# Performance work log

Measured on AMD Instinct MI355X. Metric: run time of the kernel, lower is better.

Reference implementation:

```python
import jax, jax.numpy as jnp
import numpy as np

TOP_K = 2


def setup_inputs() -> dict:
    key = jax.random.key(0)
    ks = jax.random.split(key, 6)
    B, T, H, E, F = 2, 2048, 1024, 8, 4096
    s1 = 1.0 / np.sqrt(H)
    s2 = 1.0 / np.sqrt(F)
    return {
        "hidden_states": jax.random.normal(ks[0], (B, T, H), dtype=jnp.float32),
        "router_w": jax.random.normal(ks[1], (E, H), dtype=jnp.float32) * s1,
        "w1": jax.random.normal(ks[2], (E, H, F), dtype=jnp.float32) * s1,
        "b1": jnp.zeros((E, F), dtype=jnp.float32),
        "w2": jax.random.normal(ks[3], (E, F, H), dtype=jnp.float32) * s2,
        "b2": jnp.zeros((E, H), dtype=jnp.float32),
    }


def reference(hidden_states, router_w, w1, b1, w2, b2):
    # hidden_states: [B,T,H]; router_w: [E,H]; w1: [E,H,F]; w2: [E,F,H]
    E = router_w.shape[0]
    K = TOP_K
    dt = hidden_states.dtype

    # Router
    router_logits = jnp.einsum("bth,eh->bte", hidden_states, router_w)  # [B,T,E]
    topk_values, topk_indices = jax.lax.top_k(router_logits, K)         # [B,T,K]
    topk_weights = jax.nn.softmax(topk_values.astype(jnp.float32), axis=-1).astype(dt)

    # Dense all-expert MLP (module computes every expert on every token)
    h_mid = jax.nn.gelu(
        jnp.einsum("bth,ehf->btef", hidden_states, w1) + b1, approximate=False
    )  # [B,T,E,F]
    expert_outputs = jnp.einsum("btef,efh->bteh", h_mid, w2) + b2  # [B,T,E,H]

    # Gather top-K expert outputs and combine
    topk_out = jnp.take_along_axis(expert_outputs, topk_indices[..., None], axis=2)  # [B,T,K,H]
    mixed_output = jnp.sum(topk_out * topk_weights[..., None], axis=2)  # [B,T,H]

    # Load-balancing aux loss
    router_probs = jax.nn.softmax(router_logits.astype(jnp.float32), axis=-1)
    P = router_probs.mean(axis=(0, 1))                       # [E]
    hard = jax.nn.one_hot(topk_indices, E, dtype=jnp.float32)  # [B,T,K,E]
    f = hard.mean(axis=(0, 1, 2))                            # [E]
    aux_loss = jnp.float32(E) * jnp.sum(f * P)

    # concept_mat is None in a fresh module -> statement loss is exactly 0
    statement_loss = jnp.float32(0.0)
    return mixed_output, aux_loss, statement_loss
```

## Files before the change

kernel.cpp:

```cpp
#include <hip/hip_runtime.h>


typedef unsigned short ushort_t;
typedef __attribute__((ext_vector_type(2))) float f32x2;
typedef __attribute__((ext_vector_type(4))) unsigned int u32x4;
typedef __attribute__((ext_vector_type(4))) unsigned short u16x4;
typedef __attribute__((ext_vector_type(4))) float f32x4;
typedef __attribute__((ext_vector_type(8))) __bf16 bf16x8;

#define NTOK 4096
#define HD   1024
#define FD   4096
#define NE   8
#define NKTOT 8192

__device__ __forceinline__ ushort_t f2bf(float f) {
  unsigned u = __builtin_bit_cast(unsigned, f);
  u += 0x7fffu + ((u >> 16) & 1u);
  return (ushort_t)(u >> 16);
}
__device__ __forceinline__ unsigned pk2(float a, float b) {
  unsigned r;
  asm("v_cvt_pk_bf16_f32 %0, %1, %2" : "=v"(r) : "v"(a), "v"(b));
  return r;
}
__device__ __forceinline__ float bf2f(ushort_t u) {
  unsigned v = ((unsigned)u) << 16;
  return __builtin_bit_cast(float, v);
}
__device__ __forceinline__ bf16x8 frag_ld(const void* p) {
  u32x4 v = *reinterpret_cast<const u32x4*>(p);
  return __builtin_bit_cast(bf16x8, v);
}

#define GLOAD16(g, l) __builtin_amdgcn_global_load_lds(                         \
    (const __attribute__((address_space(1))) unsigned int*)(g),                 \
    (__attribute__((address_space(3))) unsigned int*)(l), 16, 0, 0)

#define WAITLGKM() do { asm volatile("s_waitcnt lgkmcnt(0)" ::: "memory");      \
                        __builtin_amdgcn_sched_barrier(0); } while (0)
#define WAITVM0()  asm volatile("s_waitcnt vmcnt(0)" ::: "memory")
#define BARRIER() do { asm volatile("s_waitcnt lgkmcnt(0)" ::: "memory");       \
                       __builtin_amdgcn_s_barrier(); } while (0)

__global__ void init_k(int* counts) {
  if (threadIdx.x < NE) counts[threadIdx.x] = 0;
}

__global__ void convx_k(const float* __restrict__ src, ushort_t* __restrict__ dst) {
  const size_t i = ((size_t)blockIdx.x * 256 + threadIdx.x) * 4;
  const f32x4 v = *reinterpret_cast<const f32x4*>(src + i);
  u16x4 o;
  o.x = f2bf(v.x); o.y = f2bf(v.y); o.z = f2bf(v.z); o.w = f2bf(v.w);
  *reinterpret_cast<u16x4*>(dst + i) = o;
}

__global__ void router_k(const float* __restrict__ x, const float* __restrict__ rw,
                         float* __restrict__ tokP, int* __restrict__ counts,
                         int* __restrict__ tk_e, int* __restrict__ tk_s,
                         float* __restrict__ tk_w) {
  const int w = threadIdx.x >> 6, l = threadIdx.x & 63;
  const int t = blockIdx.x * 4 + w;
  const float* xr = x + (size_t)t * HD;
  float acc[NE];
#pragma unroll
  for (int e = 0; e < NE; ++e) acc[e] = 0.f;
  for (int it = 0; it < HD / 64; ++it) {
    const int h = l + it * 64;
    const float xv = xr[h];
#pragma unroll
    for (int e = 0; e < NE; ++e) acc[e] = fmaf(xv, rw[e * HD + h], acc[e]);
  }
#pragma unroll
  for (int e = 0; e < NE; ++e) {
#pragma unroll
    for (int s = 32; s > 0; s >>= 1) acc[e] += __shfl_xor(acc[e], s, 64);
  }
  float m = acc[0];
#pragma unroll
  for (int e = 1; e < NE; ++e) m = fmaxf(m, acc[e]);
  float ssum = 0.f;
  float p[NE];
#pragma unroll
  for (int e = 0; e < NE; ++e) { p[e] = expf(acc[e] - m); ssum += p[e]; }
  const float inv = 1.f / ssum;
  if (l < NE) tokP[(size_t)t * NE + l] = p[l] * inv;

  if (l == 0) {
    int i0 = 0; float v0 = acc[0];
#pragma unroll
    for (int e = 1; e < NE; ++e) if (acc[e] > v0) { v0 = acc[e]; i0 = e; }
    int i1 = -1; float v1 = -3.4e38f;
#pragma unroll
    for (int e = 0; e < NE; ++e) if (e != i0 && acc[e] > v1) { v1 = acc[e]; i1 = e; }
    const float w0 = 1.f / (1.f + expf(v1 - v0));
    const int s0 = atomicAdd(&counts[i0], 1);
    const int s1 = atomicAdd(&counts[i1], 1);
    tk_e[2 * t] = i0;     tk_s[2 * t] = s0;     tk_w[2 * t] = w0;
    tk_e[2 * t + 1] = i1; tk_s[2 * t + 1] = s1; tk_w[2 * t + 1] = 1.f - w0;
  }
}

__global__ void finalize_k(const float* __restrict__ tokP, const int* __restrict__ counts,
                           int* __restrict__ offsets, float* __restrict__ out_tail) {
  __shared__ float red[16][8];
  const int tid = threadIdx.x;
  f32x4 a0 = {0.f, 0.f, 0.f, 0.f}, a1 = {0.f, 0.f, 0.f, 0.f};
#pragma unroll
  for (int k = 0; k < 4; ++k) {
    const float* p = tokP + ((size_t)tid * 4 + k) * 8;
    a0 += *reinterpret_cast<const f32x4*>(p);
    a1 += *reinterpret_cast<const f32x4*>(p + 4);
  }
#pragma unroll
  for (int s = 1; s < 64; s <<= 1) {
#pragma unroll
    for (int c = 0; c < 4; ++c) {
      a0[c] += __shfl_xor(a0[c], s, 64);
      a1[c] += __shfl_xor(a1[c], s, 64);
    }
  }
  if ((tid & 63) == 0) {
    const int wv = tid >> 6;
#pragma unroll
    for (int c = 0; c < 4; ++c) { red[wv][c] = a0[c]; red[wv][4 + c] = a1[c]; }
  }
  __syncthreads();
  if (tid == 0) {
    float P[8];
    for (int c = 0; c < 8; ++c) {
      float s = 0.f;
      for (int q = 0; q < 16; ++q) s += red[q][c];
      P[c] = s * (1.f / NTOK);
    }
    int off = 0; float aux = 0.f;
    for (int q = 0; q < NE; ++q) { offsets[q] = off; off += counts[q]; }
    for (int q = 0; q < NE; ++q) aux += ((float)counts[q] / (float)NKTOT) * P[q];
    out_tail[0] = (float)NE * aux;
    out_tail[1] = 0.f;
  }
}

__global__ void build_slots_k(const int* __restrict__ tk_e, const int* __restrict__ tk_s,
                              const int* __restrict__ offsets, int* __restrict__ slot_token) {
  const int i = blockIdx.x * 256 + threadIdx.x;
  const int e = tk_e[i];
  slot_token[offsets[e] + tk_s[i]] = i >> 1;
}

template <bool IS_G1>
__global__ __launch_bounds__(256, 4) void moe_fused(
    const ushort_t* __restrict__ A, const float* __restrict__ W,
    const float* __restrict__ bias,
    const int* __restrict__ counts, const int* __restrict__ offsets,
    const int* __restrict__ slot_token,
    ushort_t* __restrict__ midout, ushort_t* __restrict__ ybuf) {
  constexpr int KDF = IS_G1 ? HD : FD;
  constexpr int WST = IS_G1 ? FD : HD;
  constexpr int NSTEP = IS_G1 ? 16 : 32;
  const int id = blockIdx.x;
  const int e = id & 7;
  const int q = id >> 3;
  const int ty = q % 10;
  const int r = q / 10;
  const int np = IS_G1 ? r : (r >> 1);
  const int ks = IS_G1 ? 0 : (r & 1);
  const int n0 = np * 128;
  const int KB = ks * 2048;
  const int cnt = counts[e];
  if (ty * 128 >= cnt) return;
  const int off = offsets[e];
  const int pos0 = off + ty * 128;
  const int rr = cnt - ty * 128;
  const int rows_rem = rr < 128 ? rr : 128;

  __shared__ __align__(16) ushort_t lds[16384];

  const int tid = threadIdx.x;
  const int w = tid >> 6, l = tid & 63;
  const int wr = w >> 1, wc = w & 1;

  const int sw = (((l & 7) ^ ((l >> 3) & 7)) << 4);
  const char* ab[4];
#pragma unroll
  for (int c = 0; c < 4; ++c) {
    const int row = c * 32 + w * 8 + (l >> 3);
    int pos = pos0 + row; if (pos > NKTOT - 1) pos = NKTOT - 1;
    const size_t ar = IS_G1 ? (size_t)slot_token[pos] : (size_t)pos;
    ab[c] = (const char*)A + (ar * KDF + KB) * 2 + sw;
  }

  const float* wB = W + (size_t)e * ((size_t)HD * FD) +
                    ((size_t)KB + 16 * w) * WST + n0 + 2 * l;

  f32x4 acc[4][4] = {};

  for (int t = 0; t < NSTEP; ++t) {
#pragma unroll
    for (int c = 0; c < 4; ++c)
      GLOAD16(ab[c] + t * 128, &lds[(c * 32 + w * 8) * 64]);
    f32x2 R[16];
    const float* p = wB + (size_t)(t * 64) * WST;
#pragma unroll
    for (int i = 0; i < 16; ++i)
      R[i] = *reinterpret_cast<const f32x2*>(p + (size_t)i * WST);
    WAITVM0();
    {
      ushort_t* d = &lds[8192 + (2 * l) * 64];
      const int k7 = l & 7;
      u32x4 v;
      v.x = pk2(R[0].x, R[1].x); v.y = pk2(R[2].x, R[3].x);
      v.z = pk2(R[4].x, R[5].x); v.w = pk2(R[6].x, R[7].x);
      *reinterpret_cast<u32x4*>(d + (((2 * w) ^ k7) << 3)) = v;
      v.x = pk2(R[8].x, R[9].x);  v.y = pk2(R[10].x, R[11].x);
      v.z = pk2(R[12].x, R[13].x); v.w = pk2(R[14].x, R[15].x);
      *reinterpret_cast<u32x4*>(d + (((2 * w + 1) ^ k7) << 3)) = v;
      ushort_t* d2 = d + 64;
      v.x = pk2(R[0].y, R[1].y); v.y = pk2(R[2].y, R[3].y);
      v.z = pk2(R[4].y, R[5].y); v.w = pk2(R[6].y, R[7].y);
      *reinterpret_cast<u32x4*>(d2 + (((2 * w) ^ k7) << 3)) = v;
      v.x = pk2(R[8].y, R[9].y);  v.y = pk2(R[10].y, R[11].y);
      v.z = pk2(R[12].y, R[13].y); v.w = pk2(R[14].y, R[15].y);
      *reinterpret_cast<u32x4*>(d2 + (((2 * w + 1) ^ k7) << 3)) = v;
    }
    BARRIER();
    {
      const int arow = wr * 64 + (l & 15);
      const int brow = wc * 64 + (l & 15);
      const int ax = l & 7;
      const int bx = (l >> 1) & 7;
      bf16x8 afr[4], bfr[4];
#pragma unroll
      for (int kk = 0; kk < 2; ++kk) {
        const int kc = kk * 4 + (l >> 4);
#pragma unroll
        for (int mm = 0; mm < 4; ++mm)
          afr[mm] = frag_ld(&lds[(arow + mm * 16) * 64 + ((kc ^ ax) << 3)]);
#pragma unroll
        for (int nn = 0; nn < 4; ++nn)
          bfr[nn] = frag_ld(&lds[8192 + (brow + nn * 16) * 64 + ((kc ^ bx) << 3)]);
        WAITLGKM();
        __builtin_amdgcn_s_setprio(1);
#pragma unroll
        for (int mm = 0; mm < 4; ++mm)
#pragma unroll
          for (int nn = 0; nn < 4; ++nn)
            acc[mm][nn] = __builtin_amdgcn_mfma_f32_16x16x32_bf16(
                afr[mm], bfr[nn], acc[mm][nn], 0, 0, 0);
        __builtin_amdgcn_s_setprio(0);
      }
    }
    BARRIER();
  }

  {
    const int lr4 = (l >> 4) * 4, lc = l & 15;
#pragma unroll
    for (int nn = 0; nn < 4; ++nn) {
      const int col = wc * 64 + nn * 16 + lc;
      const float bv = IS_G1 ? bias[(size_t)e * FD + n0 + col] : 0.f;
#pragma unroll
      for (int mm = 0; mm < 4; ++mm) {
        const int rb = wr * 64 + mm * 16 + lr4;
#pragma unroll
        for (int j = 0; j < 4; ++j) {
          float v = acc[mm][nn][j] + bv;
          if (IS_G1) v = 0.5f * v * (1.0f + erff(v * 0.70710678118654752f));
          lds[(rb + j) * 128 + col] = f2bf(v);
        }
      }
    }
    BARRIER();
#pragma unroll
    for (int p = 0; p < 8; ++p) {
      const int idx = p * 2048 + tid * 8;
      const int row = idx >> 7;
      const int col = idx & 127;
      if (row < rows_rem) {
        const u32x4 v = *reinterpret_cast<const u32x4*>(&lds[idx]);
        if (IS_G1)
          *reinterpret_cast<u32x4*>(&midout[(size_t)(pos0 + row) * FD + n0 + col]) = v;
        else
          *reinterpret_cast<u32x4*>(
              &ybuf[((size_t)ks * NKTOT + pos0 + row) * HD + n0 + col]) = v;
      }
    }
  }
}

__global__ void combine_k(const ushort_t* __restrict__ ybuf, const int* __restrict__ tk_e,
                          const int* __restrict__ tk_s, const float* __restrict__ tk_w,
                          const int* __restrict__ offsets, const float* __restrict__ b2,
                          float* __restrict__ out) {
  const int t = blockIdx.x;
  const int e0 = tk_e[2 * t], e1 = tk_e[2 * t + 1];
  const size_t p0 = (size_t)offsets[e0] + tk_s[2 * t];
  const size_t p1 = (size_t)offsets[e1] + tk_s[2 * t + 1];
  const float w0 = tk_w[2 * t], w1v = tk_w[2 * t + 1];
  const int h = threadIdx.x * 4;
  f32x4 s0 = *reinterpret_cast<const f32x4*>(b2 + (size_t)e0 * HD + h);
  f32x4 s1 = *reinterpret_cast<const f32x4*>(b2 + (size_t)e1 * HD + h);
#pragma unroll
  for (int ks = 0; ks < 2; ++ks) {
    const u16x4 a = *reinterpret_cast<const u16x4*>(
        &ybuf[((size_t)ks * NKTOT + p0) * HD + h]);
    const u16x4 b = *reinterpret_cast<const u16x4*>(
        &ybuf[((size_t)ks * NKTOT + p1) * HD + h]);
    s0.x += bf2f(a.x); s0.y += bf2f(a.y); s0.z += bf2f(a.z); s0.w += bf2f(a.w);
    s1.x += bf2f(b.x); s1.y += bf2f(b.y); s1.z += bf2f(b.z); s1.w += bf2f(b.w);
  }
  f32x4 o = s0 * w0 + s1 * w1v;
  *reinterpret_cast<f32x4*>(out + (size_t)t * HD + h) = o;
}

extern "C" void kernel_launch(void* const* d_in, const int* in_sizes, int n_in,
                              void* d_out, int out_size, void* d_ws, size_t ws_size,
                              hipStream_t stream) {
  const float* x  = (const float*)d_in[0];
  const float* rw = (const float*)d_in[1];
  const float* w1 = (const float*)d_in[2];
  const float* b1 = (const float*)d_in[3];
  const float* w2 = (const float*)d_in[4];
  const float* b2 = (const float*)d_in[5];
  float* out = (float*)d_out;

  char* ws = (char*)d_ws;
  ushort_t* Xbf  = (ushort_t*)(ws + 0);
  ushort_t* midb = (ushort_t*)(ws + 8388608);
  ushort_t* ybuf = (ushort_t*)(ws + 75497472);
  char* sm = ws + 209715200;
  int*   counts  = (int*)(sm);
  int*   offsets = (int*)(sm + 64);
  float* tokP    = (float*)(sm + 128);
  int*   tk_e    = (int*)(sm + 128 + 131072);
  int*   tk_s    = (int*)(sm + 128 + 131072 + 32768);
  float* tk_w    = (float*)(sm + 128 + 131072 + 65536);
  int*   slot_token = (int*)(sm + 128 + 131072 + 98304);

  init_k<<<1, 64, 0, stream>>>(counts);
  convx_k<<<4096, 256, 0, stream>>>(x, Xbf);
  router_k<<<1024, 256, 0, stream>>>(x, rw, tokP, counts, tk_e, tk_s, tk_w);
  finalize_k<<<1, 1024, 0, stream>>>(tokP, counts, offsets, out + (size_t)NTOK * HD);
  build_slots_k<<<32, 256, 0, stream>>>(tk_e, tk_s, offsets, slot_token);
  moe_fused<true><<<2560, 256, 0, stream>>>(
      Xbf, w1, b1, counts, offsets, slot_token, midb, (ushort_t*)nullptr);
  moe_fused<false><<<1280, 256, 0, stream>>>(
      midb, w2, b2, counts, offsets, slot_token, (ushort_t*)nullptr, ybuf);
  combine_k<<<4096, 256, 0, stream>>>(ybuf, tk_e, tk_s, tk_w, offsets, b2, out);
}
```

Baseline: 463.3 us.

## Pre-transpose expert weights to bf16 and load both GEMM operands via LDS DMA

```diff
diff --git a/kernel.cpp b/kernel.cpp
--- a/kernel.cpp
+++ b/kernel.cpp
@@ -2,7 +2,6 @@
 
 
 typedef unsigned short ushort_t;
-typedef __attribute__((ext_vector_type(2))) float f32x2;
 typedef __attribute__((ext_vector_type(4))) unsigned int u32x4;
 typedef __attribute__((ext_vector_type(4))) unsigned short u16x4;
 typedef __attribute__((ext_vector_type(4))) float f32x4;
@@ -19,11 +18,6 @@
   u += 0x7fffu + ((u >> 16) & 1u);
   return (ushort_t)(u >> 16);
 }
-__device__ __forceinline__ unsigned pk2(float a, float b) {
-  unsigned r;
-  asm("v_cvt_pk_bf16_f32 %0, %1, %2" : "=v"(r) : "v"(a), "v"(b));
-  return r;
-}
 __device__ __forceinline__ float bf2f(ushort_t u) {
   unsigned v = ((unsigned)u) << 16;
   return __builtin_bit_cast(float, v);
@@ -37,9 +31,7 @@
     (const __attribute__((address_space(1))) unsigned int*)(g),                 \
     (__attribute__((address_space(3))) unsigned int*)(l), 16, 0, 0)
 
-#define WAITLGKM() do { asm volatile("s_waitcnt lgkmcnt(0)" ::: "memory");      \
-                        __builtin_amdgcn_sched_barrier(0); } while (0)
-#define WAITVM0()  asm volatile("s_waitcnt vmcnt(0)" ::: "memory")
+#define WAITVM0() asm volatile("s_waitcnt vmcnt(0)" ::: "memory")
 #define BARRIER() do { asm volatile("s_waitcnt lgkmcnt(0)" ::: "memory");       \
                        __builtin_amdgcn_s_barrier(); } while (0)
 
@@ -47,27 +39,48 @@
   if (threadIdx.x < NE) counts[threadIdx.x] = 0;
 }
 
-__global__ void convx_k(const float* __restrict__ src, ushort_t* __restrict__ dst) {
-  const size_t i = ((size_t)blockIdx.x * 256 + threadIdx.x) * 4;
-  const f32x4 v = *reinterpret_cast<const f32x4*>(src + i);
-  u16x4 o;
-  o.x = f2bf(v.x); o.y = f2bf(v.y); o.z = f2bf(v.z); o.w = f2bf(v.w);
-  *reinterpret_cast<u16x4*>(dst + i) = o;
+__global__ void tconv_k(const float* __restrict__ src, ushort_t* __restrict__ dst,
+                        int R, int C) {
+  __shared__ float tile[64][65];
+  const size_t zb = (size_t)blockIdx.z * R * C;
+  const int r0 = blockIdx.y * 64, c0 = blockIdx.x * 64;
+  const int tid = threadIdx.x;
+  const int rl = tid >> 4, c4 = (tid & 15) * 4;
+#pragma unroll
+  for (int i = 0; i < 4; ++i) {
+    const int r = rl + i * 16;
+    const f32x4 v = *reinterpret_cast<const f32x4*>(src + zb + (size_t)(r0 + r) * C + c0 + c4);
+    tile[r][c4 + 0] = v.x; tile[r][c4 + 1] = v.y;
+    tile[r][c4 + 2] = v.z; tile[r][c4 + 3] = v.w;
+  }
+  __syncthreads();
+  const int rr0 = (tid & 15) * 4, ccl = tid >> 4;
+#pragma unroll
+  for (int i = 0; i < 4; ++i) {
+    const int cc = ccl + i * 16;
+    u16x4 o;
+    o.x = f2bf(tile[rr0 + 0][cc]); o.y = f2bf(tile[rr0 + 1][cc]);
+    o.z = f2bf(tile[rr0 + 2][cc]); o.w = f2bf(tile[rr0 + 3][cc]);
+    *reinterpret_cast<u16x4*>(dst + zb + (size_t)(c0 + cc) * R + r0 + rr0) = o;
+  }
 }
 
 __global__ void router_k(const float* __restrict__ x, const float* __restrict__ rw,
+                         ushort_t* __restrict__ Xbf,
                          float* __restrict__ tokP, int* __restrict__ counts,
                          int* __restrict__ tk_e, int* __restrict__ tk_s,
                          float* __restrict__ tk_w) {
   const int w = threadIdx.x >> 6, l = threadIdx.x & 63;
   const int t = blockIdx.x * 4 + w;
   const float* xr = x + (size_t)t * HD;
+  ushort_t* xo = Xbf + (size_t)t * HD;
   float acc[NE];
 #pragma unroll
   for (int e = 0; e < NE; ++e) acc[e] = 0.f;
   for (int it = 0; it < HD / 64; ++it) {
     const int h = l + it * 64;
     const float xv = xr[h];
+    xo[h] = f2bf(xv);
 #pragma unroll
     for (int e = 0; e < NE; ++e) acc[e] = fmaf(xv, rw[e * HD + h], acc[e]);
   }
@@ -149,14 +162,14 @@
 }
 
 template <bool IS_G1>
-__global__ __launch_bounds__(256, 4) void moe_fused(
-    const ushort_t* __restrict__ A, const float* __restrict__ W,
+__global__ __launch_bounds__(256, 4) void moe_gemm(
+    const ushort_t* __restrict__ A, const ushort_t* __restrict__ BT,
     const float* __restrict__ bias,
     const int* __restrict__ counts, const int* __restrict__ offsets,
     const int* __restrict__ slot_token,
     ushort_t* __restrict__ midout, ushort_t* __restrict__ ybuf) {
   constexpr int KDF = IS_G1 ? HD : FD;
-  constexpr int WST = IS_G1 ? FD : HD;
+  constexpr int ND  = IS_G1 ? FD : HD;
   constexpr int NSTEP = IS_G1 ? 16 : 32;
   const int id = blockIdx.x;
   const int e = id & 7;
@@ -181,72 +194,50 @@
   const int wr = w >> 1, wc = w & 1;
 
   const int sw = (((l & 7) ^ ((l >> 3) & 7)) << 4);
-  const char* ab[4];
+  const char* aptr[4];
+  const char* bptr[4];
 #pragma unroll
   for (int c = 0; c < 4; ++c) {
     const int row = c * 32 + w * 8 + (l >> 3);
     int pos = pos0 + row; if (pos > NKTOT - 1) pos = NKTOT - 1;
     const size_t ar = IS_G1 ? (size_t)slot_token[pos] : (size_t)pos;
-    ab[c] = (const char*)A + (ar * KDF + KB) * 2 + sw;
-  }
-
-  const float* wB = W + (size_t)e * ((size_t)HD * FD) +
-                    ((size_t)KB + 16 * w) * WST + n0 + 2 * l;
+    aptr[c] = (const char*)A + (ar * KDF + KB) * 2 + sw;
+    const int rb = n0 + row;
+    bptr[c] = (const char*)BT + (((size_t)e * ND + rb) * KDF + KB) * 2 + sw;
+  }
 
   f32x4 acc[4][4] = {};
 
   for (int t = 0; t < NSTEP; ++t) {
 #pragma unroll
     for (int c = 0; c < 4; ++c)
-      GLOAD16(ab[c] + t * 128, &lds[(c * 32 + w * 8) * 64]);
-    f32x2 R[16];
-    const float* p = wB + (size_t)(t * 64) * WST;
-#pragma unroll
-    for (int i = 0; i < 16; ++i)
-      R[i] = *reinterpret_cast<const f32x2*>(p + (size_t)i * WST);
+      GLOAD16(aptr[c] + t * 128, &lds[(c * 32 + w * 8) * 64]);
+#pragma unroll
+    for (int c = 0; c < 4; ++c)
+      GLOAD16(bptr[c] + t * 128, &lds[8192 + (c * 32 + w * 8) * 64]);
     WAITVM0();
-    {
-      ushort_t* d = &lds[8192 + (2 * l) * 64];
-      const int k7 = l & 7;
-      u32x4 v;
-      v.x = pk2(R[0].x, R[1].x); v.y = pk2(R[2].x, R[3].x);
-      v.z = pk2(R[4].x, R[5].x); v.w = pk2(R[6].x, R[7].x);
-      *reinterpret_cast<u32x4*>(d + (((2 * w) ^ k7) << 3)) = v;
-      v.x = pk2(R[8].x, R[9].x);  v.y = pk2(R[10].x, R[11].x);
-      v.z = pk2(R[12].x, R[13].x); v.w = pk2(R[14].x, R[15].x);
-      *reinterpret_cast<u32x4*>(d + (((2 * w + 1) ^ k7) << 3)) = v;
-      ushort_t* d2 = d + 64;
-      v.x = pk2(R[0].y, R[1].y); v.y = pk2(R[2].y, R[3].y);
-      v.z = pk2(R[4].y, R[5].y); v.w = pk2(R[6].y, R[7].y);
-      *reinterpret_cast<u32x4*>(d2 + (((2 * w) ^ k7) << 3)) = v;
-      v.x = pk2(R[8].y, R[9].y);  v.y = pk2(R[10].y, R[11].y);
-      v.z = pk2(R[12].y, R[13].y); v.w = pk2(R[14].y, R[15].y);
-      *reinterpret_cast<u32x4*>(d2 + (((2 * w + 1) ^ k7) << 3)) = v;
-    }
     BARRIER();
     {
       const int arow = wr * 64 + (l & 15);
       const int brow = wc * 64 + (l & 15);
-      const int ax = l & 7;
-      const int bx = (l >> 1) & 7;
-      bf16x8 afr[4], bfr[4];
+      const int key = l & 7;
 #pragma unroll
       for (int kk = 0; kk < 2; ++kk) {
         const int kc = kk * 4 + (l >> 4);
+        bf16x8 afr[4];
 #pragma unroll
         for (int mm = 0; mm < 4; ++mm)
-          afr[mm] = frag_ld(&lds[(arow + mm * 16) * 64 + ((kc ^ ax) << 3)]);
-#pragma unroll
-        for (int nn = 0; nn < 4; ++nn)
-          bfr[nn] = frag_ld(&lds[8192 + (brow + nn * 16) * 64 + ((kc ^ bx) << 3)]);
-        WAITLGKM();
+          afr[mm] = frag_ld(&lds[(arow + mm * 16) * 64 + ((kc ^ key) << 3)]);
         __builtin_amdgcn_s_setprio(1);
 #pragma unroll
-        for (int mm = 0; mm < 4; ++mm)
-#pragma unroll
-          for (int nn = 0; nn < 4; ++nn)
+        for (int nn = 0; nn < 4; ++nn) {
+          const bf16x8 bfr =
+              frag_ld(&lds[8192 + (brow + nn * 16) * 64 + ((kc ^ key) << 3)]);
+#pragma unroll
+          for (int mm = 0; mm < 4; ++mm)
             acc[mm][nn] = __builtin_amdgcn_mfma_f32_16x16x32_bf16(
-                afr[mm], bfr[nn], acc[mm][nn], 0, 0, 0);
+                afr[mm], bfr, acc[mm][nn], 0, 0, 0);
+        }
         __builtin_amdgcn_s_setprio(0);
       }
     }
@@ -326,8 +317,10 @@
 
   char* ws = (char*)d_ws;
   ushort_t* Xbf  = (ushort_t*)(ws + 0);
-  ushort_t* midb = (ushort_t*)(ws + 8388608);
-  ushort_t* ybuf = (ushort_t*)(ws + 75497472);
+  ushort_t* W1T  = (ushort_t*)(ws + 8388608);
+  ushort_t* W2T  = (ushort_t*)(ws + 75497472);
+  ushort_t* midb = (ushort_t*)(ws + 142606336);
+  ushort_t* ybuf = (ushort_t*)(ws + 8388608);
   char* sm = ws + 209715200;
   int*   counts  = (int*)(sm);
   int*   offsets = (int*)(sm + 64);
@@ -338,13 +331,14 @@
   int*   slot_token = (int*)(sm + 128 + 131072 + 98304);
 
   init_k<<<1, 64, 0, stream>>>(counts);
-  convx_k<<<4096, 256, 0, stream>>>(x, Xbf);
-  router_k<<<1024, 256, 0, stream>>>(x, rw, tokP, counts, tk_e, tk_s, tk_w);
+  tconv_k<<<dim3(64, 16, 8), 256, 0, stream>>>(w1, W1T, HD, FD);
+  tconv_k<<<dim3(16, 64, 8), 256, 0, stream>>>(w2, W2T, FD, HD);
+  router_k<<<1024, 256, 0, stream>>>(x, rw, Xbf, tokP, counts, tk_e, tk_s, tk_w);
   finalize_k<<<1, 1024, 0, stream>>>(tokP, counts, offsets, out + (size_t)NTOK * HD);
   build_slots_k<<<32, 256, 0, stream>>>(tk_e, tk_s, offsets, slot_token);
-  moe_fused<true><<<2560, 256, 0, stream>>>(
-      Xbf, w1, b1, counts, offsets, slot_token, midb, (ushort_t*)nullptr);
-  moe_fused<false><<<1280, 256, 0, stream>>>(
-      midb, w2, b2, counts, offsets, slot_token, (ushort_t*)nullptr, ybuf);
+  moe_gemm<true><<<2560, 256, 0, stream>>>(
+      Xbf, W1T, b1, counts, offsets, slot_token, midb, (ushort_t*)nullptr);
+  moe_gemm<false><<<1280, 256, 0, stream>>>(
+      midb, W2T, b2, counts, offsets, slot_token, (ushort_t*)nullptr, ybuf);
   combine_k<<<4096, 256, 0, stream>>>(ybuf, tk_e, tk_s, tk_w, offsets, b2, out);
 }
```

New measurement: 414.5 us. 1.12x faster.
